# Performance work log

Hardware: AMD Instinct MI355X
Metric: run time of the kernel (lower is better)

The kernel has to match this reference:

```python
import jax, jax.numpy as jnp
import numpy as np

N_USERS = 40000
N_ITEMS = 20000
D = 128
N_EDGES = 320000
LAYERS = 3
EPS = 1e-7
BATCH = 4096


def setup_inputs() -> dict:
    key = jax.random.key(0)
    k1, k2, k3, k4, k5, k6, k7 = jax.random.split(key, 7)
    user_emb = jax.random.normal(k1, (N_USERS, D), jnp.float32) * 0.02
    item_emb = jax.random.normal(k2, (N_ITEMS, D), jnp.float32) * 0.02
    adj_user = jax.random.randint(k3, (N_EDGES,), 0, N_USERS)
    adj_item = jax.random.randint(k4, (N_EDGES,), 0, N_ITEMS)
    user = jax.random.randint(k5, (BATCH,), 0, N_USERS)
    # items are 1-indexed in the original forward (pos_item - 1)
    pos_item = jax.random.randint(k6, (BATCH,), 1, N_ITEMS + 1)
    neg_item = jax.random.randint(k7, (BATCH,), 1, N_ITEMS + 1)
    return dict(user_emb=user_emb, item_emb=item_emb,
                adj_user=adj_user, adj_item=adj_item,
                user=user, pos_item=pos_item, neg_item=neg_item)


def _norm_adj(adj_user, adj_item):
    # Symmetric bipartite adjacency A over (U+I) nodes with D^-1/2 A D^-1/2 norm.
    N = N_USERS + N_ITEMS
    rows = jnp.concatenate([adj_user, adj_item + N_USERS])
    cols = jnp.concatenate([adj_item + N_USERS, adj_user])
    deg = jnp.zeros((N,), jnp.float32).at[rows].add(1.0) + EPS  # (A>0).sum(1)+eps
    dinv = deg ** -0.5
    vals = dinv[rows] * dinv[cols]  # interaction values are 1.0
    return rows, cols, vals


def _encode(user_emb, item_emb, rows, cols, vals):
    N = N_USERS + N_ITEMS
    x = jnp.concatenate([user_emb, item_emb], axis=0)  # [N, D]
    acc = x
    for _ in range(LAYERS):
        # SpMM: out[r] += v_e * x[c] for each edge e=(r,c)
        x = jax.ops.segment_sum(vals[:, None] * x[cols], rows, num_segments=N)
        acc = acc + x
    all_emb = acc / jnp.float32(LAYERS + 1)  # mean over layer outputs
    return all_emb[:N_USERS], all_emb[N_USERS:]


def reference(user_emb, item_emb, adj_user, adj_item, user, pos_item, neg_item):
    rows, cols, vals = _norm_adj(adj_user, adj_item)
    u_lat, i_lat = _encode(user_emb, item_emb, rows, cols, vals)
    tu = u_lat[user]                  # [B, D]
    pi = i_lat[pos_item - 1]          # [B, D]
    ni = i_lat[neg_item - 1]          # [B, D]
    pos_scores = jnp.sum(tu * pi, axis=-1)
    neg_scores = jnp.sum(tu * ni, axis=-1)
    # BPR loss: -mean(log sigmoid(pos - neg))
    loss = -jnp.mean(jax.nn.log_sigmoid(pos_scores - neg_scores))
    return loss
```

## Files before the change

### kernel.cpp

```cpp
#include <hip/hip_runtime.h>
#include <math.h>

#define N_USERS 40000
#define N_ITEMS 20000
#define NNODES  60000
#define D       128
#define N_EDGES 320000
#define EPS_    1e-7f
#define BATCH   4096
#define STRIDE  64
#define ZSCALE  256.0f
#define BPR_BLOCKS (BATCH / 8)
#define FILL_GRPS  320
#define FILL_BLOCKS (8 * FILL_GRPS)
#define INIT_BLOCKS (((NNODES + 1) * 16 + 255) / 256)
#define FULL_BLOCKS (NNODES * 8 / 256)

typedef float vf2 __attribute__((ext_vector_type(2)));

__device__ __forceinline__ void add_fp8x16v(vf2* a, uint4 t) {
    a[0] += __builtin_amdgcn_cvt_pk_f32_fp8(t.x, false);
    a[1] += __builtin_amdgcn_cvt_pk_f32_fp8(t.x, true);
    a[2] += __builtin_amdgcn_cvt_pk_f32_fp8(t.y, false);
    a[3] += __builtin_amdgcn_cvt_pk_f32_fp8(t.y, true);
    a[4] += __builtin_amdgcn_cvt_pk_f32_fp8(t.z, false);
    a[5] += __builtin_amdgcn_cvt_pk_f32_fp8(t.z, true);
    a[6] += __builtin_amdgcn_cvt_pk_f32_fp8(t.w, false);
    a[7] += __builtin_amdgcn_cvt_pk_f32_fp8(t.w, true);
}

__device__ __forceinline__ uint4 pack_fp8x16v(const vf2* a, float w) {
    float v[16];
    #pragma unroll
    for (int k = 0; k < 8; ++k) {
        v[2 * k]     = fminf(fmaxf(w * a[k].x, -448.0f), 448.0f);
        v[2 * k + 1] = fminf(fmaxf(w * a[k].y, -448.0f), 448.0f);
    }
    int w0 = __builtin_amdgcn_cvt_pk_fp8_f32(v[0],  v[1],  0,  false);
    w0     = __builtin_amdgcn_cvt_pk_fp8_f32(v[2],  v[3],  w0, true);
    int w1 = __builtin_amdgcn_cvt_pk_fp8_f32(v[4],  v[5],  0,  false);
    w1     = __builtin_amdgcn_cvt_pk_fp8_f32(v[6],  v[7],  w1, true);
    int w2 = __builtin_amdgcn_cvt_pk_fp8_f32(v[8],  v[9],  0,  false);
    w2     = __builtin_amdgcn_cvt_pk_fp8_f32(v[10], v[11], w2, true);
    int w3 = __builtin_amdgcn_cvt_pk_fp8_f32(v[12], v[13], 0,  false);
    w3     = __builtin_amdgcn_cvt_pk_fp8_f32(v[14], v[15], w3, true);
    uint4 o; o.x = (unsigned)w0; o.y = (unsigned)w1;
    o.z = (unsigned)w2; o.w = (unsigned)w3;
    return o;
}

__device__ __forceinline__ void gather8(const int4* __restrict__ rcv, int t,
                                        const uint4* __restrict__ z, int sub,
                                        vf2* a) {
    int4 ca = rcv[2 * t], cb = rcv[2 * t + 1];
    uint4 t0 = z[(ca.x << 3) + sub];
    uint4 t1 = z[(ca.y << 3) + sub];
    uint4 t2 = z[(ca.z << 3) + sub];
    uint4 t3 = z[(ca.w << 3) + sub];
    uint4 t4 = z[(cb.x << 3) + sub];
    uint4 t5 = z[(cb.y << 3) + sub];
    uint4 t6 = z[(cb.z << 3) + sub];
    uint4 t7 = z[(cb.w << 3) + sub];
    add_fp8x16v(a, t0); add_fp8x16v(a, t1);
    add_fp8x16v(a, t2); add_fp8x16v(a, t3);
    add_fp8x16v(a, t4); add_fp8x16v(a, t5);
    add_fp8x16v(a, t6); add_fp8x16v(a, t7);
}

__global__ void fill_ell(const int2* __restrict__ au2, const int2* __restrict__ ai2,
                         int* __restrict__ fillc, int* __restrict__ colell) {
    const int bucket = blockIdx.x & 7;
    const int grp    = blockIdx.x >> 3;
    const int NE2    = N_EDGES / 2;
    for (int i = grp * 256 + threadIdx.x; i < NE2; i += FILL_GRPS * 256) {
        int2 us = au2[i];
        int2 is = ai2[i];
        int u0 = us.x, i0 = N_USERS + is.x;
        int u1 = us.y, i1 = N_USERS + is.y;
        if (u0 / 10000 == bucket) {
            int pos = atomicAdd(&fillc[u0], 1);
            if (pos < STRIDE) colell[(u0 << 6) + pos] = i0;
        }
        if (u1 / 10000 == bucket) {
            int pos = atomicAdd(&fillc[u1], 1);
            if (pos < STRIDE) colell[(u1 << 6) + pos] = i1;
        }
        if (4 + (i0 - N_USERS) / 5000 == bucket) {
            int pos = atomicAdd(&fillc[i0], 1);
            if (pos < STRIDE) colell[(i0 << 6) + pos] = u0;
        }
        if (4 + (i1 - N_USERS) / 5000 == bucket) {
            int pos = atomicAdd(&fillc[i1], 1);
            if (pos < STRIDE) colell[(i1 << 6) + pos] = u1;
        }
    }
}

__global__ void init_z(const int* __restrict__ fillc,
                       const float4* __restrict__ ue, const float4* __restrict__ ie,
                       uint2* __restrict__ z0, uint2* __restrict__ z1,
                       uint2* __restrict__ z2, int* __restrict__ colell) {
    int i   = blockIdx.x * 256 + threadIdx.x;
    if (i >= (NNODES + 1) * 16) return;
    int row = i >> 4;
    int sub = i & 15;
    if (row == NNODES) {
        uint2 zz = make_uint2(0u, 0u);
        z0[i] = zz; z1[i] = zz; z2[i] = zz;
        return;
    }
    int e = fillc[row];
    if (sub == 0) {
        int ep = (e + 7) & ~7;
        for (int k = e; k < ep; ++k) colell[(row << 6) + k] = NNODES;
    }
    float w = rsqrtf((float)e + EPS_) * ZSCALE;
    float4 e0, e1;
    if (row < N_USERS) {
        int b4 = row * 32 + sub * 2;
        e0 = ue[b4]; e1 = ue[b4 + 1];
    } else {
        int b4 = (row - N_USERS) * 32 + sub * 2;
        e0 = ie[b4]; e1 = ie[b4 + 1];
    }
    float v[8] = { e0.x * w, e0.y * w, e0.z * w, e0.w * w,
                   e1.x * w, e1.y * w, e1.z * w, e1.w * w };
    float c[8];
    #pragma unroll
    for (int k = 0; k < 8; ++k) c[k] = fminf(fmaxf(v[k], -448.0f), 448.0f);
    int lo = __builtin_amdgcn_cvt_pk_fp8_f32(c[0], c[1], 0,  false);
    lo     = __builtin_amdgcn_cvt_pk_fp8_f32(c[2], c[3], lo, true);
    int hi = __builtin_amdgcn_cvt_pk_fp8_f32(c[4], c[5], 0,  false);
    hi     = __builtin_amdgcn_cvt_pk_fp8_f32(c[6], c[7], hi, true);
    z0[i] = make_uint2((unsigned)lo, (unsigned)hi);
}

__device__ __forceinline__ void spmm_body(const int* __restrict__ cnt,
                                          const int* __restrict__ colell,
                                          const uint4* __restrict__ z,
                                          uint4* __restrict__ znxt) {
    int tid = blockIdx.x * 256 + threadIdx.x;
    int row = tid >> 3;
    int sub = threadIdx.x & 7;
    int e = cnt[row];
    const int4* rcv = (const int4*)(colell + (row << 6));
    vf2 a[8];
    #pragma unroll
    for (int k = 0; k < 8; ++k) a[k] = (vf2)(0.0f);
    int nchunks = (e + 7) >> 3;
    for (int t = 0; t < nchunks; ++t) gather8(rcv, t, z, sub, a);
    float w = 1.0f / ((float)e + EPS_);
    znxt[(row << 3) + sub] = pack_fp8x16v(a, w);
}

__global__ void spmm_L1(const int* __restrict__ cnt, const int* __restrict__ colell,
                        const uint4* __restrict__ z, uint4* __restrict__ znxt) {
    spmm_body(cnt, colell, z, znxt);
}
__global__ void spmm_L2(const int* __restrict__ cnt, const int* __restrict__ colell,
                        const uint4* __restrict__ z, uint4* __restrict__ znxt) {
    spmm_body(cnt, colell, z, znxt);
}

__global__ void bpr_loss(const float4* __restrict__ ue, const float4* __restrict__ ie,
                         const uint4* __restrict__ z1, const uint4* __restrict__ z2,
                         const int* __restrict__ cnt, const int* __restrict__ colell,
                         const int* __restrict__ user, const int* __restrict__ pos,
                         const int* __restrict__ neg,
                         float* __restrict__ lacc, int* __restrict__ done,
                         float* __restrict__ out) {
    __shared__ float s[8];
    int wave = (blockIdx.x * 256 + threadIdx.x) >> 6;
    int lane = threadIdx.x & 63;
    int sg   = lane >> 3;
    int sub  = lane & 7;
    int half = sg >> 2;
    int sgl  = sg & 3;
    int el   = wave * 2 + half;
    int u = user[el];
    int p = N_USERS + pos[el] - 1;
    int n = N_USERS + neg[el] - 1;
    int node = (sgl == 1) ? p : (sgl == 2) ? n : u;
    float cnode = 0.0f;
    vf2 vals[8];
    #pragma unroll
    for (int k = 0; k < 8; ++k) vals[k] = (vf2)(0.0f);
    if (sgl < 3) {
        int e = cnt[node];
        cnode = (float)e;
        const float4* eb = (node < N_USERS) ? ue : ie;
        int b4 = ((node < N_USERS) ? node : node - N_USERS) * 32 + sub * 4;
        float4 e0 = eb[b4], e1 = eb[b4 + 1], e2 = eb[b4 + 2], e3 = eb[b4 + 3];
        float w0 = rsqrtf(cnode + EPS_) * ZSCALE;
        vals[0] = (vf2){w0 * e0.x, w0 * e0.y}; vals[1] = (vf2){w0 * e0.z, w0 * e0.w};
        vals[2] = (vf2){w0 * e1.x, w0 * e1.y}; vals[3] = (vf2){w0 * e1.z, w0 * e1.w};
        vals[4] = (vf2){w0 * e2.x, w0 * e2.y}; vals[5] = (vf2){w0 * e2.z, w0 * e2.w};
        vals[6] = (vf2){w0 * e3.x, w0 * e3.y}; vals[7] = (vf2){w0 * e3.z, w0 * e3.w};
        int o = (node << 3) + sub;
        add_fp8x16v(vals, z1[o]);
        add_fp8x16v(vals, z2[o]);
        const int4* rcv = (const int4*)(colell + (node << 6));
        vf2 a[8];
        #pragma unroll
        for (int k = 0; k < 8; ++k) a[k] = (vf2)(0.0f);
        int nchunks = (e + 7) >> 3;
        for (int t = 0; t < nchunks; ++t) gather8(rcv, t, z2, sub, a);
        float w2 = 1.0f / (cnode + EPS_);
        #pragma unroll
        for (int k = 0; k < 8; ++k) vals[k] += w2 * a[k];
    }
    int usrc = sub | (lane & 32);
    float dotp = 0.0f;
    #pragma unroll
    for (int k = 0; k < 8; ++k) {
        dotp += __shfl(vals[k].x, usrc) * vals[k].x;
        dotp += __shfl(vals[k].y, usrc) * vals[k].y;
    }
    dotp += __shfl_down(dotp, 4, 8);
    dotp += __shfl_down(dotp, 2, 8);
    dotp += __shfl_down(dotp, 1, 8);
    float sp = __shfl(dotp, (lane & 32) + 8);
    float sn = __shfl(dotp, (lane & 32) + 16);
    float cu = __shfl(cnode, (lane & 32) + 0);
    float cp = __shfl(cnode, (lane & 32) + 8);
    float cn = __shfl(cnode, (lane & 32) + 16);
    if ((lane & 31) == 0) {
        float du = rsqrtf(cu + EPS_), dp = rsqrtf(cp + EPS_), dn = rsqrtf(cn + EPS_);
        const float inv = 1.0f / (16.0f * ZSCALE * ZSCALE);
        float diff = (sp / (du * dp) - sn / (du * dn)) * inv;
        s[(threadIdx.x >> 6) * 2 + half] =
            fminf(diff, 0.0f) - log1pf(expf(-fabsf(diff)));
    }
    __syncthreads();
    if (threadIdx.x == 0) {
        float t = s[0] + s[1] + s[2] + s[3] + s[4] + s[5] + s[6] + s[7];
        atomicAdd(lacc, t);
        __threadfence();
        int prev = atomicAdd(done, 1);
        if (prev == BPR_BLOCKS - 1) {
            float total = atomicAdd(lacc, 0.0f);
            out[0] = -total * (1.0f / (float)BATCH);
        }
    }
}

extern "C" void kernel_launch(void* const* d_in, const int* in_sizes, int n_in,
                              void* d_out, int out_size, void* d_ws, size_t ws_size,
                              hipStream_t stream) {
    const float* ue  = (const float*)d_in[0];
    const float* ie  = (const float*)d_in[1];
    const int*   au  = (const int*)d_in[2];
    const int*   ai  = (const int*)d_in[3];
    const int*   usr = (const int*)d_in[4];
    const int*   pos = (const int*)d_in[5];
    const int*   neg = (const int*)d_in[6];
    float*       out = (float*)d_out;

    const size_t ZQ4 = (size_t)(NNODES + 1) * 8;

    uint4* z0     = (uint4*)d_ws;
    uint4* z1     = z0 + ZQ4;
    uint4* z2     = z1 + ZQ4;
    int*   fillc  = (int*)(z2 + ZQ4);
    float* lacc   = (float*)(fillc + NNODES);
    int*   done   = (int*)(lacc + 1);
    int*   colell = (int*)(lacc + 4);

    hipMemsetAsync(fillc, 0, (NNODES + 4) * sizeof(int), stream);

    fill_ell<<<FILL_BLOCKS, 256, 0, stream>>>((const int2*)au, (const int2*)ai,
                                              fillc, colell);
    init_z<<<INIT_BLOCKS, 256, 0, stream>>>(fillc, (const float4*)ue,
                                            (const float4*)ie, (uint2*)z0,
                                            (uint2*)z1, (uint2*)z2, colell);

    spmm_L1<<<FULL_BLOCKS, 256, 0, stream>>>(fillc, colell, z0, z1);
    spmm_L2<<<FULL_BLOCKS, 256, 0, stream>>>(fillc, colell, z1, z2);

    bpr_loss<<<BPR_BLOCKS, 256, 0, stream>>>((const float4*)ue, (const float4*)ie,
                                             z1, z2, fillc, colell,
                                             usr, pos, neg, lacc, done, out);
}
```

Measured before the change: 162.6 us.

## Fuse all phases into one persistent kernel with software grid barriers

Replaces the five separate launches (ELL fill, init, two SpMM layers, BPR loss) with one persistent kernel sized to occupancy, separated by atomic-counter grid barriers. Each phase becomes a grid-stride loop, and the fill phase now reads edges as int4. The goal is to remove per-launch overhead and the gaps between kernels. The cost is barrier spin latency and fewer resident blocks for the latency-bound gathers, plus deadlock risk if not all blocks are co-resident.

```diff
diff --git a/kernel.cpp b/kernel.cpp
--- a/kernel.cpp
+++ b/kernel.cpp
@@ -10,11 +10,7 @@
 #define BATCH   4096
 #define STRIDE  64
 #define ZSCALE  256.0f
-#define BPR_BLOCKS (BATCH / 8)
-#define FILL_GRPS  320
-#define FILL_BLOCKS (8 * FILL_GRPS)
-#define INIT_BLOCKS (((NNODES + 1) * 16 + 255) / 256)
-#define FULL_BLOCKS (NNODES * 8 / 256)
+#define MAX_NB  1024
 
 typedef float vf2 __attribute__((ext_vector_type(2)));
 
@@ -67,180 +63,214 @@
     add_fp8x16v(a, t6); add_fp8x16v(a, t7);
 }
 
-__global__ void fill_ell(const int2* __restrict__ au2, const int2* __restrict__ ai2,
-                         int* __restrict__ fillc, int* __restrict__ colell) {
+__device__ __forceinline__ void gbar(int* bcnt, int* bgen, int nb) {
+    __syncthreads();
+    if (threadIdx.x == 0) {
+        __threadfence();
+        int g = __hip_atomic_load(bgen, __ATOMIC_RELAXED, __HIP_MEMORY_SCOPE_AGENT);
+        int a = __hip_atomic_fetch_add(bcnt, 1, __ATOMIC_ACQ_REL,
+                                       __HIP_MEMORY_SCOPE_AGENT);
+        if (a == nb - 1) {
+            __hip_atomic_store(bcnt, 0, __ATOMIC_RELAXED, __HIP_MEMORY_SCOPE_AGENT);
+            __hip_atomic_fetch_add(bgen, 1, __ATOMIC_RELEASE,
+                                   __HIP_MEMORY_SCOPE_AGENT);
+        } else {
+            while (__hip_atomic_load(bgen, __ATOMIC_ACQUIRE,
+                                     __HIP_MEMORY_SCOPE_AGENT) == g)
+                __builtin_amdgcn_s_sleep(2);
+        }
+    }
+    __syncthreads();
+}
+
+__device__ __forceinline__ void fill_phase(const int4* __restrict__ au4,
+                                           const int4* __restrict__ ai4,
+                                           int* __restrict__ fillc,
+                                           int* __restrict__ colell, int nb) {
     const int bucket = blockIdx.x & 7;
-    const int grp    = blockIdx.x >> 3;
-    const int NE2    = N_EDGES / 2;
-    for (int i = grp * 256 + threadIdx.x; i < NE2; i += FILL_GRPS * 256) {
-        int2 us = au2[i];
-        int2 is = ai2[i];
-        int u0 = us.x, i0 = N_USERS + is.x;
-        int u1 = us.y, i1 = N_USERS + is.y;
-        if (u0 / 10000 == bucket) {
-            int pos = atomicAdd(&fillc[u0], 1);
-            if (pos < STRIDE) colell[(u0 << 6) + pos] = i0;
-        }
-        if (u1 / 10000 == bucket) {
-            int pos = atomicAdd(&fillc[u1], 1);
-            if (pos < STRIDE) colell[(u1 << 6) + pos] = i1;
-        }
-        if (4 + (i0 - N_USERS) / 5000 == bucket) {
-            int pos = atomicAdd(&fillc[i0], 1);
-            if (pos < STRIDE) colell[(i0 << 6) + pos] = u0;
-        }
-        if (4 + (i1 - N_USERS) / 5000 == bucket) {
-            int pos = atomicAdd(&fillc[i1], 1);
-            if (pos < STRIDE) colell[(i1 << 6) + pos] = u1;
-        }
-    }
-}
-
-__global__ void init_z(const int* __restrict__ fillc,
-                       const float4* __restrict__ ue, const float4* __restrict__ ie,
-                       uint2* __restrict__ z0, uint2* __restrict__ z1,
-                       uint2* __restrict__ z2, int* __restrict__ colell) {
-    int i   = blockIdx.x * 256 + threadIdx.x;
-    if (i >= (NNODES + 1) * 16) return;
-    int row = i >> 4;
-    int sub = i & 15;
-    if (row == NNODES) {
-        uint2 zz = make_uint2(0u, 0u);
-        z0[i] = zz; z1[i] = zz; z2[i] = zz;
-        return;
-    }
-    int e = fillc[row];
-    if (sub == 0) {
-        int ep = (e + 7) & ~7;
-        for (int k = e; k < ep; ++k) colell[(row << 6) + k] = NNODES;
-    }
-    float w = rsqrtf((float)e + EPS_) * ZSCALE;
-    float4 e0, e1;
-    if (row < N_USERS) {
-        int b4 = row * 32 + sub * 2;
-        e0 = ue[b4]; e1 = ue[b4 + 1];
-    } else {
-        int b4 = (row - N_USERS) * 32 + sub * 2;
-        e0 = ie[b4]; e1 = ie[b4 + 1];
-    }
-    float v[8] = { e0.x * w, e0.y * w, e0.z * w, e0.w * w,
-                   e1.x * w, e1.y * w, e1.z * w, e1.w * w };
-    float c[8];
-    #pragma unroll
-    for (int k = 0; k < 8; ++k) c[k] = fminf(fmaxf(v[k], -448.0f), 448.0f);
-    int lo = __builtin_amdgcn_cvt_pk_fp8_f32(c[0], c[1], 0,  false);
-    lo     = __builtin_amdgcn_cvt_pk_fp8_f32(c[2], c[3], lo, true);
-    int hi = __builtin_amdgcn_cvt_pk_fp8_f32(c[4], c[5], 0,  false);
-    hi     = __builtin_amdgcn_cvt_pk_fp8_f32(c[6], c[7], hi, true);
-    z0[i] = make_uint2((unsigned)lo, (unsigned)hi);
-}
-
-__device__ __forceinline__ void spmm_body(const int* __restrict__ cnt,
-                                          const int* __restrict__ colell,
-                                          const uint4* __restrict__ z,
-                                          uint4* __restrict__ znxt) {
-    int tid = blockIdx.x * 256 + threadIdx.x;
-    int row = tid >> 3;
-    int sub = threadIdx.x & 7;
-    int e = cnt[row];
-    const int4* rcv = (const int4*)(colell + (row << 6));
-    vf2 a[8];
-    #pragma unroll
-    for (int k = 0; k < 8; ++k) a[k] = (vf2)(0.0f);
-    int nchunks = (e + 7) >> 3;
-    for (int t = 0; t < nchunks; ++t) gather8(rcv, t, z, sub, a);
-    float w = 1.0f / ((float)e + EPS_);
-    znxt[(row << 3) + sub] = pack_fp8x16v(a, w);
-}
-
-__global__ void spmm_L1(const int* __restrict__ cnt, const int* __restrict__ colell,
-                        const uint4* __restrict__ z, uint4* __restrict__ znxt) {
-    spmm_body(cnt, colell, z, znxt);
-}
-__global__ void spmm_L2(const int* __restrict__ cnt, const int* __restrict__ colell,
-                        const uint4* __restrict__ z, uint4* __restrict__ znxt) {
-    spmm_body(cnt, colell, z, znxt);
-}
-
-__global__ void bpr_loss(const float4* __restrict__ ue, const float4* __restrict__ ie,
-                         const uint4* __restrict__ z1, const uint4* __restrict__ z2,
-                         const int* __restrict__ cnt, const int* __restrict__ colell,
-                         const int* __restrict__ user, const int* __restrict__ pos,
-                         const int* __restrict__ neg,
-                         float* __restrict__ lacc, int* __restrict__ done,
-                         float* __restrict__ out) {
-    __shared__ float s[8];
-    int wave = (blockIdx.x * 256 + threadIdx.x) >> 6;
-    int lane = threadIdx.x & 63;
-    int sg   = lane >> 3;
-    int sub  = lane & 7;
-    int half = sg >> 2;
-    int sgl  = sg & 3;
-    int el   = wave * 2 + half;
-    int u = user[el];
-    int p = N_USERS + pos[el] - 1;
-    int n = N_USERS + neg[el] - 1;
-    int node = (sgl == 1) ? p : (sgl == 2) ? n : u;
-    float cnode = 0.0f;
-    vf2 vals[8];
-    #pragma unroll
-    for (int k = 0; k < 8; ++k) vals[k] = (vf2)(0.0f);
-    if (sgl < 3) {
-        int e = cnt[node];
-        cnode = (float)e;
-        const float4* eb = (node < N_USERS) ? ue : ie;
-        int b4 = ((node < N_USERS) ? node : node - N_USERS) * 32 + sub * 4;
-        float4 e0 = eb[b4], e1 = eb[b4 + 1], e2 = eb[b4 + 2], e3 = eb[b4 + 3];
-        float w0 = rsqrtf(cnode + EPS_) * ZSCALE;
-        vals[0] = (vf2){w0 * e0.x, w0 * e0.y}; vals[1] = (vf2){w0 * e0.z, w0 * e0.w};
-        vals[2] = (vf2){w0 * e1.x, w0 * e1.y}; vals[3] = (vf2){w0 * e1.z, w0 * e1.w};
-        vals[4] = (vf2){w0 * e2.x, w0 * e2.y}; vals[5] = (vf2){w0 * e2.z, w0 * e2.w};
-        vals[6] = (vf2){w0 * e3.x, w0 * e3.y}; vals[7] = (vf2){w0 * e3.z, w0 * e3.w};
-        int o = (node << 3) + sub;
-        add_fp8x16v(vals, z1[o]);
-        add_fp8x16v(vals, z2[o]);
-        const int4* rcv = (const int4*)(colell + (node << 6));
+    const int stride = (nb >> 3) * 256;
+    const int NE4 = N_EDGES / 4;
+    for (int i = (blockIdx.x >> 3) * 256 + threadIdx.x; i < NE4; i += stride) {
+        int4 us = au4[i];
+        int4 is = ai4[i];
+        int ua[4] = { us.x, us.y, us.z, us.w };
+        int ia[4] = { is.x, is.y, is.z, is.w };
+        #pragma unroll
+        for (int k = 0; k < 4; ++k) {
+            int u    = ua[k];
+            int iraw = ia[k];
+            int it   = N_USERS + iraw;
+            if (u / 10000 == bucket) {
+                int p = atomicAdd(&fillc[u], 1);
+                if (p < STRIDE) colell[(u << 6) + p] = it;
+            }
+            if (4 + iraw / 5000 == bucket) {
+                int p = atomicAdd(&fillc[it], 1);
+                if (p < STRIDE) colell[(it << 6) + p] = u;
+            }
+        }
+    }
+}
+
+__device__ __forceinline__ void init_phase(const int* __restrict__ fillc,
+        const float4* __restrict__ ue, const float4* __restrict__ ie,
+        uint2* __restrict__ z0, uint2* __restrict__ z1, uint2* __restrict__ z2,
+        int* __restrict__ colell, int nb) {
+    const int total = (NNODES + 1) * 16;
+    for (int i = blockIdx.x * 256 + threadIdx.x; i < total; i += nb * 256) {
+        int row = i >> 4;
+        int sub = i & 15;
+        if (row == NNODES) {
+            uint2 zz = make_uint2(0u, 0u);
+            z0[i] = zz; z1[i] = zz; z2[i] = zz;
+            continue;
+        }
+        int e = fillc[row];
+        if (sub == 0) {
+            int ep = (e + 7) & ~7;
+            for (int k = e; k < ep; ++k) colell[(row << 6) + k] = NNODES;
+        }
+        float w = rsqrtf((float)e + EPS_) * ZSCALE;
+        float4 e0, e1;
+        if (row < N_USERS) {
+            int b4 = row * 32 + sub * 2;
+            e0 = ue[b4]; e1 = ue[b4 + 1];
+        } else {
+            int b4 = (row - N_USERS) * 32 + sub * 2;
+            e0 = ie[b4]; e1 = ie[b4 + 1];
+        }
+        float v[8] = { e0.x * w, e0.y * w, e0.z * w, e0.w * w,
+                       e1.x * w, e1.y * w, e1.z * w, e1.w * w };
+        float c[8];
+        #pragma unroll
+        for (int k = 0; k < 8; ++k) c[k] = fminf(fmaxf(v[k], -448.0f), 448.0f);
+        int lo = __builtin_amdgcn_cvt_pk_fp8_f32(c[0], c[1], 0,  false);
+        lo     = __builtin_amdgcn_cvt_pk_fp8_f32(c[2], c[3], lo, true);
+        int hi = __builtin_amdgcn_cvt_pk_fp8_f32(c[4], c[5], 0,  false);
+        hi     = __builtin_amdgcn_cvt_pk_fp8_f32(c[6], c[7], hi, true);
+        z0[i] = make_uint2((unsigned)lo, (unsigned)hi);
+    }
+}
+
+__device__ __forceinline__ void spmm_phase(const int* __restrict__ cnt,
+        const int* __restrict__ colell, const uint4* __restrict__ z,
+        uint4* __restrict__ znxt, int nb) {
+    const int sub = threadIdx.x & 7;
+    for (int base = blockIdx.x * 32; base < NNODES; base += nb * 32) {
+        int row = base + (threadIdx.x >> 3);
+        int e = cnt[row];
+        const int4* rcv = (const int4*)(colell + (row << 6));
         vf2 a[8];
         #pragma unroll
         for (int k = 0; k < 8; ++k) a[k] = (vf2)(0.0f);
         int nchunks = (e + 7) >> 3;
-        for (int t = 0; t < nchunks; ++t) gather8(rcv, t, z2, sub, a);
-        float w2 = 1.0f / (cnode + EPS_);
-        #pragma unroll
-        for (int k = 0; k < 8; ++k) vals[k] += w2 * a[k];
-    }
-    int usrc = sub | (lane & 32);
-    float dotp = 0.0f;
-    #pragma unroll
-    for (int k = 0; k < 8; ++k) {
-        dotp += __shfl(vals[k].x, usrc) * vals[k].x;
-        dotp += __shfl(vals[k].y, usrc) * vals[k].y;
-    }
-    dotp += __shfl_down(dotp, 4, 8);
-    dotp += __shfl_down(dotp, 2, 8);
-    dotp += __shfl_down(dotp, 1, 8);
-    float sp = __shfl(dotp, (lane & 32) + 8);
-    float sn = __shfl(dotp, (lane & 32) + 16);
-    float cu = __shfl(cnode, (lane & 32) + 0);
-    float cp = __shfl(cnode, (lane & 32) + 8);
-    float cn = __shfl(cnode, (lane & 32) + 16);
-    if ((lane & 31) == 0) {
-        float du = rsqrtf(cu + EPS_), dp = rsqrtf(cp + EPS_), dn = rsqrtf(cn + EPS_);
-        const float inv = 1.0f / (16.0f * ZSCALE * ZSCALE);
-        float diff = (sp / (du * dp) - sn / (du * dn)) * inv;
-        s[(threadIdx.x >> 6) * 2 + half] =
-            fminf(diff, 0.0f) - log1pf(expf(-fabsf(diff)));
-    }
+        for (int t = 0; t < nchunks; ++t) gather8(rcv, t, z, sub, a);
+        float w = 1.0f / ((float)e + EPS_);
+        znxt[(row << 3) + sub] = pack_fp8x16v(a, w);
+    }
+}
+
+__device__ __forceinline__ void bpr_phase(
+        const float4* __restrict__ ue, const float4* __restrict__ ie,
+        const uint4* __restrict__ z1, const uint4* __restrict__ z2,
+        const int* __restrict__ cnt, const int* __restrict__ colell,
+        const int* __restrict__ user, const int* __restrict__ pos,
+        const int* __restrict__ neg, float* __restrict__ lacc, int nb) {
+    __shared__ float s[8];
+    if (threadIdx.x < 8) s[threadIdx.x] = 0.0f;
+    __syncthreads();
+    const int lane = threadIdx.x & 63;
+    const int sg   = lane >> 3;
+    const int sub  = lane & 7;
+    const int half = sg >> 2;
+    const int sgl  = sg & 3;
+    float lsum = 0.0f;
+    for (int w = blockIdx.x * 4 + (int)(threadIdx.x >> 6); w < BATCH / 2;
+         w += nb * 4) {
+        int el = w * 2 + half;
+        int u = user[el];
+        int p = N_USERS + pos[el] - 1;
+        int n = N_USERS + neg[el] - 1;
+        int node = (sgl == 1) ? p : (sgl == 2) ? n : u;
+        float cnode = 0.0f;
+        vf2 vals[8];
+        #pragma unroll
+        for (int k = 0; k < 8; ++k) vals[k] = (vf2)(0.0f);
+        if (sgl < 3) {
+            int e = cnt[node];
+            cnode = (float)e;
+            const float4* eb = (node < N_USERS) ? ue : ie;
+            int b4 = ((node < N_USERS) ? node : node - N_USERS) * 32 + sub * 4;
+            float4 e0 = eb[b4], e1 = eb[b4 + 1], e2 = eb[b4 + 2], e3 = eb[b4 + 3];
+            float w0 = rsqrtf(cnode + EPS_) * ZSCALE;
+            vals[0] = (vf2){w0 * e0.x, w0 * e0.y}; vals[1] = (vf2){w0 * e0.z, w0 * e0.w};
+            vals[2] = (vf2){w0 * e1.x, w0 * e1.y}; vals[3] = (vf2){w0 * e1.z, w0 * e1.w};
+            vals[4] = (vf2){w0 * e2.x, w0 * e2.y}; vals[5] = (vf2){w0 * e2.z, w0 * e2.w};
+            vals[6] = (vf2){w0 * e3.x, w0 * e3.y}; vals[7] = (vf2){w0 * e3.z, w0 * e3.w};
+            int o = (node << 3) + sub;
+            add_fp8x16v(vals, z1[o]);
+            add_fp8x16v(vals, z2[o]);
+            const int4* rcv = (const int4*)(colell + (node << 6));
+            vf2 a[8];
+            #pragma unroll
+            for (int k = 0; k < 8; ++k) a[k] = (vf2)(0.0f);
+            int nchunks = (e + 7) >> 3;
+            for (int t = 0; t < nchunks; ++t) gather8(rcv, t, z2, sub, a);
+            float w2 = 1.0f / (cnode + EPS_);
+            #pragma unroll
+            for (int k = 0; k < 8; ++k) vals[k] += w2 * a[k];
+        }
+        int usrc = sub | (lane & 32);
+        float dotp = 0.0f;
+        #pragma unroll
+        for (int k = 0; k < 8; ++k) {
+            dotp += __shfl(vals[k].x, usrc) * vals[k].x;
+            dotp += __shfl(vals[k].y, usrc) * vals[k].y;
+        }
+        dotp += __shfl_down(dotp, 4, 8);
+        dotp += __shfl_down(dotp, 2, 8);
+        dotp += __shfl_down(dotp, 1, 8);
+        float sp = __shfl(dotp, (lane & 32) + 8);
+        float sn = __shfl(dotp, (lane & 32) + 16);
+        float cu = __shfl(cnode, (lane & 32) + 0);
+        float cp = __shfl(cnode, (lane & 32) + 8);
+        float cn = __shfl(cnode, (lane & 32) + 16);
+        if ((lane & 31) == 0) {
+            float du = rsqrtf(cu + EPS_), dp = rsqrtf(cp + EPS_), dn = rsqrtf(cn + EPS_);
+            const float inv = 1.0f / (16.0f * ZSCALE * ZSCALE);
+            float diff = (sp / (du * dp) - sn / (du * dn)) * inv;
+            lsum += fminf(diff, 0.0f) - log1pf(expf(-fabsf(diff)));
+        }
+    }
+    if ((lane & 31) == 0) s[(threadIdx.x >> 6) * 2 + half] = lsum;
     __syncthreads();
     if (threadIdx.x == 0) {
         float t = s[0] + s[1] + s[2] + s[3] + s[4] + s[5] + s[6] + s[7];
         atomicAdd(lacc, t);
-        __threadfence();
-        int prev = atomicAdd(done, 1);
-        if (prev == BPR_BLOCKS - 1) {
-            float total = atomicAdd(lacc, 0.0f);
-            out[0] = -total * (1.0f / (float)BATCH);
-        }
+    }
+}
+
+__global__ void __launch_bounds__(256)
+lightgcn_mega(const float4* ue, const float4* ie,
+              const int* au, const int* ai,
+              const int* user, const int* pos, const int* neg,
+              uint4* z0, uint4* z1, uint4* z2,
+              int* fillc, int* colell, float* lacc,
+              int* bcnt, int* bgen, float* out, int nb) {
+    fill_phase((const int4*)au, (const int4*)ai, fillc, colell, nb);
+    gbar(bcnt, bgen, nb);
+    init_phase(fillc, ue, ie, (uint2*)z0, (uint2*)z1, (uint2*)z2, colell, nb);
+    gbar(bcnt, bgen, nb);
+    spmm_phase(fillc, colell, z0, z1, nb);
+    gbar(bcnt, bgen, nb);
+    spmm_phase(fillc, colell, z1, z2, nb);
+    gbar(bcnt, bgen, nb);
+    bpr_phase(ue, ie, z1, z2, fillc, colell, user, pos, neg, lacc, nb);
+    gbar(bcnt, bgen, nb);
+    if (blockIdx.x == 0 && threadIdx.x == 0) {
+        float total = __hip_atomic_load(lacc, __ATOMIC_RELAXED,
+                                        __HIP_MEMORY_SCOPE_AGENT);
+        out[0] = -total * (1.0f / (float)BATCH);
     }
 }
 
@@ -263,21 +293,36 @@
     uint4* z2     = z1 + ZQ4;
     int*   fillc  = (int*)(z2 + ZQ4);
     float* lacc   = (float*)(fillc + NNODES);
-    int*   done   = (int*)(lacc + 1);
+    int*   bcnt   = (int*)(lacc + 1);
+    int*   bgen   = bcnt + 1;
     int*   colell = (int*)(lacc + 4);
 
+    static int nb = 0;
+    if (nb == 0) {
+        int mob = 0;
+        hipError_t err = hipOccupancyMaxActiveBlocksPerMultiprocessor(
+            &mob, lightgcn_mega, 256, 0);
+        long t;
+        if (err != hipSuccess || mob <= 0) {
+            t = 256;
+        } else {
+            hipDeviceProp_t prop;
+            int dev = 0;
+            (void)hipGetDevice(&dev);
+            if (hipGetDeviceProperties(&prop, dev) == hipSuccess)
+                t = (long)mob * (long)prop.multiProcessorCount;
+            else
+                t = 256;
+        }
+        if (t > MAX_NB) t = MAX_NB;
+        t &= ~7L;
+        if (t < 8) t = 8;
+        nb = (int)t;
+    }
+
     hipMemsetAsync(fillc, 0, (NNODES + 4) * sizeof(int), stream);
 
-    fill_ell<<<FILL_BLOCKS, 256, 0, stream>>>((const int2*)au, (const int2*)ai,
-                                              fillc, colell);
-    init_z<<<INIT_BLOCKS, 256, 0, stream>>>(fillc, (const float4*)ue,
-                                            (const float4*)ie, (uint2*)z0,
-                                            (uint2*)z1, (uint2*)z2, colell);
-
-    spmm_L1<<<FULL_BLOCKS, 256, 0, stream>>>(fillc, colell, z0, z1);
-    spmm_L2<<<FULL_BLOCKS, 256, 0, stream>>>(fillc, colell, z1, z2);
-
-    bpr_loss<<<BPR_BLOCKS, 256, 0, stream>>>((const float4*)ue, (const float4*)ie,
-                                             z1, z2, fillc, colell,
-                                             usr, pos, neg, lacc, done, out);
-}
+    lightgcn_mega<<<nb, 256, 0, stream>>>(
+        (const float4*)ue, (const float4*)ie, au, ai, usr, pos, neg,
+        z0, z1, z2, fillc, colell, lacc, bcnt, bgen, out, nb);
+}
```

After: 574.5 us. +253.4%, slower.
